# Kernel tuning notes

Hardware: AMD Instinct MI355X
Metric: run time of the kernel (lower is better)

The kernel has to match this reference:

```python
import jax, jax.numpy as jnp
import numpy as np

HIDDEN = 10

def setup_inputs() -> dict:
    key = jax.random.key(0)
    ks = jax.random.split(key, 12)
    B, T = 4096, 2048
    s_in = 1.0 / np.sqrt(HIDDEN)  # PyTorch RNN/Linear default init scale
    inp = {
        "x": jax.random.normal(ks[0], (B, T, 1), dtype=jnp.float32),
        "hidden_state": jax.random.normal(ks[1], (2, B, HIDDEN), dtype=jnp.float32),
        # layer 0 (input_size=1)
        "W_ih0": jax.random.uniform(ks[2], (HIDDEN, 1), jnp.float32, -s_in, s_in),
        "W_hh0": jax.random.uniform(ks[3], (HIDDEN, HIDDEN), jnp.float32, -s_in, s_in),
        "b_ih0": jax.random.uniform(ks[4], (HIDDEN,), jnp.float32, -s_in, s_in),
        "b_hh0": jax.random.uniform(ks[5], (HIDDEN,), jnp.float32, -s_in, s_in),
        # layer 1 (input_size=HIDDEN)
        "W_ih1": jax.random.uniform(ks[6], (HIDDEN, HIDDEN), jnp.float32, -s_in, s_in),
        "W_hh1": jax.random.uniform(ks[7], (HIDDEN, HIDDEN), jnp.float32, -s_in, s_in),
        "b_ih1": jax.random.uniform(ks[8], (HIDDEN,), jnp.float32, -s_in, s_in),
        "b_hh1": jax.random.uniform(ks[9], (HIDDEN,), jnp.float32, -s_in, s_in),
        # output Linear(10, 1)
        "W_out": jax.random.uniform(ks[10], (1, HIDDEN), jnp.float32, -s_in, s_in),
        "b_out": jax.random.uniform(ks[11], (1,), jnp.float32, -s_in, s_in),
    }
    return inp


def reference(x, hidden_state, W_ih0, W_hh0, b_ih0, b_hh0,
              W_ih1, W_hh1, b_ih1, b_hh1, W_out, b_out):
    # x: [B, T, 1]; hidden_state: [2, B, H]
    h0_init, h1_init = hidden_state[0], hidden_state[1]  # [B, H] each
    xs = jnp.swapaxes(x, 0, 1)  # [T, B, 1] for scan over time

    def step(carry, xt):
        h0, h1 = carry
        h0n = jnp.tanh(xt @ W_ih0.T + b_ih0 + h0 @ W_hh0.T + b_hh0)
        h1n = jnp.tanh(h0n @ W_ih1.T + b_ih1 + h1 @ W_hh1.T + b_hh1)
        return (h0n, h1n), h1n

    (h0_f, h1_f), ys = jax.lax.scan(step, (h0_init, h1_init), xs)  # ys: [T, B, H]
    rnn_output = jnp.swapaxes(ys, 0, 1)  # [B, T, H]
    outs = rnn_output @ W_out.T + b_out  # [B, T, 1] (fused per-timestep Linear)
    hidden_out = jnp.stack([h0_f, h1_f], axis=0)  # [2, B, H]
    return outs, hidden_out
```

## Files before the change

kernel.cpp:

```cpp
#include <hip/hip_runtime.h>

#define HID 10
#define TT  2048
#define BB  4096

typedef float f2 __attribute__((ext_vector_type(2)));

static __device__ __forceinline__ f2 pkmul(f2 a, f2 b) {
    f2 d; asm("v_pk_mul_f32 %0, %1, %2" : "=v"(d) : "v"(a), "v"(b)); return d;
}
static __device__ __forceinline__ f2 pkfma(f2 a, f2 b, f2 c) {
    f2 d; asm("v_pk_fma_f32 %0, %1, %2, %3" : "=v"(d) : "v"(a), "v"(b), "v"(c)); return d;
}

__device__ __forceinline__ float fast_tanh(float x) {
    float e = exp2f(x * 2.885390081777926814f);
    float r = __builtin_amdgcn_rcpf(e + 1.0f);
    return fmaf(-2.0f, r, 1.0f);
}

__global__ void __launch_bounds__(128) rnn_kernel(
    const float* __restrict__ x,    const float* __restrict__ hs,
    const float* __restrict__ Wih0, const float* __restrict__ Whh0,
    const float* __restrict__ bih0, const float* __restrict__ bhh0,
    const float* __restrict__ Wih1, const float* __restrict__ Whh1,
    const float* __restrict__ bih1, const float* __restrict__ bhh1,
    const float* __restrict__ Wout, const float* __restrict__ boutp,
    float* __restrict__ out)
{
    const int tid   = threadIdx.x;
    const bool isA  = tid < 64;
    const int lane  = tid & 15;
    const int grp   = (tid >> 4) & 3;
    const int row   = blockIdx.x * 4 + grp;
    const bool act  = (lane < HID);
    const bool olane = (lane == HID);

    __shared__ float lds[4 * 144];
    float* ring = &lds[grp * 144];
    float* h1b  = &lds[grp * 144 + 128];

    const float* xrow = x   + (size_t)row * TT;
    float*       orow = out + (size_t)row * TT;

    f2 whh0p[5]; float wih0i = 0.f, b0c = 0.f;
    f2 H0[5];
    float4 xq = make_float4(0.f, 0.f, 0.f, 0.f);
    float h0own = 0.f;
    f2 wih1p[5], whh1p[5]; float b1c = 0.f;
    f2 H1[5];
    float h1own = 0.f;
    float P1 = 0.f, P2 = 0.f, P3 = 0.f;

    if (isA) {
        #pragma unroll
        for (int j = 0; j < 5; ++j)
            whh0p[j] = act ? f2{Whh0[lane*HID + 2*j], Whh0[lane*HID + 2*j+1]}
                           : f2{0.f, 0.f};
        wih0i = act ? Wih0[lane] : 0.f;
        b0c   = act ? (bih0[lane] + bhh0[lane]) : 0.f;
        #pragma unroll
        for (int j = 0; j < 5; ++j)
            H0[j] = f2{hs[row*HID + 2*j], hs[row*HID + 2*j+1]};
        xq = *(const float4*)(xrow);
    } else {
        #pragma unroll
        for (int j = 0; j < 5; ++j) {
            wih1p[j] = act ? f2{Wih1[lane*HID + 2*j], Wih1[lane*HID + 2*j+1]}
                           : f2{0.f, 0.f};
            whh1p[j] = act ? f2{Whh1[lane*HID + 2*j], Whh1[lane*HID + 2*j+1]}
                     : (olane ? f2{Wout[2*j], Wout[2*j+1]} : f2{0.f, 0.f});
        }
        b1c = act ? (bih1[lane] + bhh1[lane]) : (olane ? boutp[0] : 0.f);
        #pragma unroll
        for (int j = 0; j < 5; ++j)
            H1[j] = f2{hs[BB*HID + row*HID + 2*j], hs[BB*HID + row*HID + 2*j+1]};
    }

    for (int m = 0; m <= TT / 4; ++m) {
        if (isA) {
            if (m < TT / 4) {
                const int mn = (m + 1 < TT / 4) ? m + 1 : m;
                const float4 xn = *(const float4*)(xrow + 4 * mn);
                const float xs[4] = {xq.x, xq.y, xq.z, xq.w};
                #pragma unroll
                for (int k = 0; k < 4; ++k) {
                    const int i = 4 * m + k;
                    f2 acc = pkmul(whh0p[0], H0[0]);
                    acc = pkfma(whh0p[1], H0[1], acc);
                    acc = pkfma(whh0p[2], H0[2], acc);
                    acc = pkfma(whh0p[3], H0[3], acc);
                    acc = pkfma(whh0p[4], H0[4], acc);
                    const float a0 = fmaf(xs[k], wih0i, b0c);
                    h0own = fast_tanh((a0 + acc.x) + acc.y);
                    ring[(i & 7) * 16 + lane] = h0own;
                    __builtin_amdgcn_wave_barrier();
                    const float* rb = &ring[(i & 7) * 16];
                    const float4 r0 = *(const float4*)(rb);
                    const float4 r1 = *(const float4*)(rb + 4);
                    const f2     r2 = *(const f2*)(rb + 8);
                    H0[0] = f2{r0.x, r0.y}; H0[1] = f2{r0.z, r0.w};
                    H0[2] = f2{r1.x, r1.y}; H0[3] = f2{r1.z, r1.w};
                    H0[4] = r2;
                }
                xq = xn;
            }
        } else {
            if (m > 0) {
                const int tb = 4 * (m - 1);
                f2 hb[4][5];
                #pragma unroll
                for (int k = 0; k < 4; ++k) {
                    const float* rb = &ring[((tb + k) & 7) * 16];
                    const float4 r0 = *(const float4*)(rb);
                    const float4 r1 = *(const float4*)(rb + 4);
                    const f2     r2 = *(const f2*)(rb + 8);
                    hb[k][0] = f2{r0.x, r0.y}; hb[k][1] = f2{r0.z, r0.w};
                    hb[k][2] = f2{r1.x, r1.y}; hb[k][3] = f2{r1.z, r1.w};
                    hb[k][4] = r2;
                }
                float c0 = 0.f, c1 = 0.f, c2 = 0.f, c3 = 0.f;
                #pragma unroll
                for (int k = 0; k < 4; ++k) {
                    f2 bcc = pkmul(wih1p[0], hb[k][0]);
                    bcc = pkfma(wih1p[1], hb[k][1], bcc);
                    bcc = pkfma(wih1p[2], hb[k][2], bcc);
                    bcc = pkfma(wih1p[3], hb[k][3], bcc);
                    bcc = pkfma(wih1p[4], hb[k][4], bcc);
                    bcc = pkfma(whh1p[0], H1[0], bcc);
                    bcc = pkfma(whh1p[1], H1[1], bcc);
                    bcc = pkfma(whh1p[2], H1[2], bcc);
                    bcc = pkfma(whh1p[3], H1[3], bcc);
                    bcc = pkfma(whh1p[4], H1[4], bcc);
                    const float s1 = (b1c + bcc.x) + bcc.y;
                    if      (k == 0) c0 = s1;
                    else if (k == 1) c1 = s1;
                    else if (k == 2) c2 = s1;
                    else             c3 = s1;
                    h1own = fast_tanh(s1);
                    h1b[lane] = h1own;
                    __builtin_amdgcn_wave_barrier();
                    const float4 q0 = *(const float4*)(h1b);
                    const float4 q1 = *(const float4*)(h1b + 4);
                    const f2     q2 = *(const f2*)(h1b + 8);
                    H1[0] = f2{q0.x, q0.y}; H1[1] = f2{q0.z, q0.w};
                    H1[2] = f2{q1.x, q1.y}; H1[3] = f2{q1.z, q1.w};
                    H1[4] = q2;
                }
                if (olane && m >= 2)
                    *(float4*)(orow + tb - 4) = make_float4(P1, P2, P3, c0);
                P1 = c1; P2 = c2; P3 = c3;
            }
        }
        __syncthreads();
    }

    if (!isA) {
        f2 cc = pkmul(whh1p[0], H1[0]);
        cc = pkfma(whh1p[1], H1[1], cc);
        cc = pkfma(whh1p[2], H1[2], cc);
        cc = pkfma(whh1p[3], H1[3], cc);
        cc = pkfma(whh1p[4], H1[4], cc);
        const float ofin = (b1c + cc.x) + cc.y;
        if (olane)
            *(float4*)(orow + TT - 4) = make_float4(P1, P2, P3, ofin);
    }

    if (isA) {
        if (act) out[(size_t)BB*TT + (size_t)row*HID + lane] = h0own;
    } else {
        if (act) out[(size_t)BB*TT + (size_t)BB*HID + (size_t)row*HID + lane] = h1own;
    }
}

extern "C" void kernel_launch(void* const* d_in, const int* in_sizes, int n_in,
                              void* d_out, int out_size, void* d_ws, size_t ws_size,
                              hipStream_t stream) {
    const float* x    = (const float*)d_in[0];
    const float* hs   = (const float*)d_in[1];
    const float* Wih0 = (const float*)d_in[2];
    const float* Whh0 = (const float*)d_in[3];
    const float* bih0 = (const float*)d_in[4];
    const float* bhh0 = (const float*)d_in[5];
    const float* Wih1 = (const float*)d_in[6];
    const float* Whh1 = (const float*)d_in[7];
    const float* bih1 = (const float*)d_in[8];
    const float* bhh1 = (const float*)d_in[9];
    const float* Wout = (const float*)d_in[10];
    const float* bout = (const float*)d_in[11];
    float* out = (float*)d_out;

    dim3 grid(BB / 4), block(128);
    hipLaunchKernelGGL(rnn_kernel, grid, block, 0, stream,
        x, hs, Wih0, Whh0, bih0, bhh0, Wih1, Whh1, bih1, bhh1, Wout, bout, out);
}
```

Baseline: 298.1 us.

## Interleave two independent batch rows per thread group to hide recurrence latency

Each 16-lane group now advances two batch rows instead of one, interleaving their serial recurrence steps so that the dependency chains (packed FMAs, tanh, LDS exchange) of one row can overlap with the other's. The grid is halved and the LDS ring buffers are doubled to match. This is meant to raise instruction-level parallelism in a latency-bound sequential loop, at the cost of more registers per thread and half as many blocks in flight.

```diff
diff --git a/kernel.cpp b/kernel.cpp
--- a/kernel.cpp
+++ b/kernel.cpp
@@ -32,25 +32,28 @@
     const bool isA  = tid < 64;
     const int lane  = tid & 15;
     const int grp   = (tid >> 4) & 3;
-    const int row   = blockIdx.x * 4 + grp;
+    const int row0  = blockIdx.x * 8 + grp;
+    const int row1  = row0 + 4;
     const bool act  = (lane < HID);
     const bool olane = (lane == HID);
 
-    __shared__ float lds[4 * 144];
-    float* ring = &lds[grp * 144];
-    float* h1b  = &lds[grp * 144 + 128];
-
-    const float* xrow = x   + (size_t)row * TT;
-    float*       orow = out + (size_t)row * TT;
-
-    f2 whh0p[5]; float wih0i = 0.f, b0c = 0.f;
-    f2 H0[5];
-    float4 xq = make_float4(0.f, 0.f, 0.f, 0.f);
-    float h0own = 0.f;
-    f2 wih1p[5], whh1p[5]; float b1c = 0.f;
-    f2 H1[5];
-    float h1own = 0.f;
-    float P1 = 0.f, P2 = 0.f, P3 = 0.f;
+    __shared__ float lds[8 * 144];
+    float* ring0 = &lds[grp * 144];
+    float* ring1 = &lds[(grp + 4) * 144];
+    float* h1b0  = ring0 + 128;
+    float* h1b1  = ring1 + 128;
+
+    const float* x0 = x + (size_t)row0 * TT;
+    const float* x1 = x + (size_t)row1 * TT;
+    float*       o0 = out + (size_t)row0 * TT;
+    float*       o1 = out + (size_t)row1 * TT;
+
+    f2 whh0p[5]; float wih0i = 0.f, bc = 0.f;
+    f2 wih1p[5], whh1p[5];
+    f2 H_0[5], H_1[5];
+    float4 xq0 = make_float4(0,0,0,0), xq1 = make_float4(0,0,0,0);
+    float own0 = 0.f, own1 = 0.f;
+    float P10=0.f,P20=0.f,P30=0.f, P11=0.f,P21=0.f,P31=0.f;
 
     if (isA) {
         #pragma unroll
@@ -58,11 +61,14 @@
             whh0p[j] = act ? f2{Whh0[lane*HID + 2*j], Whh0[lane*HID + 2*j+1]}
                            : f2{0.f, 0.f};
         wih0i = act ? Wih0[lane] : 0.f;
-        b0c   = act ? (bih0[lane] + bhh0[lane]) : 0.f;
-        #pragma unroll
-        for (int j = 0; j < 5; ++j)
-            H0[j] = f2{hs[row*HID + 2*j], hs[row*HID + 2*j+1]};
-        xq = *(const float4*)(xrow);
+        bc    = act ? (bih0[lane] + bhh0[lane]) : 0.f;
+        #pragma unroll
+        for (int j = 0; j < 5; ++j) {
+            H_0[j] = f2{hs[row0*HID + 2*j], hs[row0*HID + 2*j+1]};
+            H_1[j] = f2{hs[row1*HID + 2*j], hs[row1*HID + 2*j+1]};
+        }
+        xq0 = *(const float4*)(x0);
+        xq1 = *(const float4*)(x1);
     } else {
         #pragma unroll
         for (int j = 0; j < 5; ++j) {
@@ -71,106 +77,139 @@
             whh1p[j] = act ? f2{Whh1[lane*HID + 2*j], Whh1[lane*HID + 2*j+1]}
                      : (olane ? f2{Wout[2*j], Wout[2*j+1]} : f2{0.f, 0.f});
         }
-        b1c = act ? (bih1[lane] + bhh1[lane]) : (olane ? boutp[0] : 0.f);
-        #pragma unroll
-        for (int j = 0; j < 5; ++j)
-            H1[j] = f2{hs[BB*HID + row*HID + 2*j], hs[BB*HID + row*HID + 2*j+1]};
-    }
-
-    for (int m = 0; m <= TT / 4; ++m) {
+        bc = act ? (bih1[lane] + bhh1[lane]) : (olane ? boutp[0] : 0.f);
+        #pragma unroll
+        for (int j = 0; j < 5; ++j) {
+            H_0[j] = f2{hs[BB*HID + row0*HID + 2*j], hs[BB*HID + row0*HID + 2*j+1]};
+            H_1[j] = f2{hs[BB*HID + row1*HID + 2*j], hs[BB*HID + row1*HID + 2*j+1]};
+        }
+    }
+
+#define ASTEP(HV, RING, XV, OWN) do {                                    \
+    f2 acc = pkmul(whh0p[0], HV[0]);                                     \
+    acc = pkfma(whh0p[1], HV[1], acc);                                   \
+    acc = pkfma(whh0p[2], HV[2], acc);                                   \
+    acc = pkfma(whh0p[3], HV[3], acc);                                   \
+    acc = pkfma(whh0p[4], HV[4], acc);                                   \
+    const float a0 = fmaf((XV), wih0i, bc);                              \
+    OWN = fast_tanh((a0 + acc.x) + acc.y);                               \
+    (RING)[slot + lane] = OWN;                                           \
+    __builtin_amdgcn_wave_barrier();                                     \
+    const float* _rb = (RING) + slot;                                    \
+    const float4 _r0 = *(const float4*)(_rb);                            \
+    const float4 _r1 = *(const float4*)(_rb + 4);                        \
+    const f2     _r2 = *(const f2*)(_rb + 8);                            \
+    HV[0] = f2{_r0.x, _r0.y}; HV[1] = f2{_r0.z, _r0.w};                  \
+    HV[2] = f2{_r1.x, _r1.y}; HV[3] = f2{_r1.z, _r1.w};                  \
+    HV[4] = _r2;                                                         \
+} while (0)
+
+#define BSTEP(HV, H1B, U0, U1, U2, OWN, SDST) do {                       \
+    f2 qc = pkmul(whh1p[0], HV[0]);                                      \
+    qc = pkfma(whh1p[1], HV[1], qc);                                     \
+    qc = pkfma(whh1p[2], HV[2], qc);                                     \
+    qc = pkfma(whh1p[3], HV[3], qc);                                     \
+    qc = pkfma(whh1p[4], HV[4], qc);                                     \
+    f2 pc = pkmul(wih1p[0], f2{U0.x, U0.y});                             \
+    pc = pkfma(wih1p[1], f2{U0.z, U0.w}, pc);                            \
+    pc = pkfma(wih1p[2], f2{U1.x, U1.y}, pc);                            \
+    pc = pkfma(wih1p[3], f2{U1.z, U1.w}, pc);                            \
+    pc = pkfma(wih1p[4], U2, pc);                                        \
+    const float _s1 = ((bc + qc.x) + qc.y) + (pc.x + pc.y);              \
+    SDST = _s1;                                    \
+    OWN = fast_tanh(_s1);                                                \
+    (H1B)[lane] = OWN;                                                   \
+    __builtin_amdgcn_wave_barrier();                                     \
+    const float4 _q0 = *(const float4*)(H1B);                            \
+    const float4 _q1 = *(const float4*)((H1B) + 4);                      \
+    const f2     _q2 = *(const f2*)((H1B) + 8);                          \
+    HV[0] = f2{_q0.x, _q0.y}; HV[1] = f2{_q0.z, _q0.w};                  \
+    HV[2] = f2{_q1.x, _q1.y}; HV[3] = f2{_q1.z, _q1.w};                  \
+    HV[4] = _q2;                                                         \
+} while (0)
+
+    const int M = TT / 4;
+    for (int m = 0; m <= M; ++m) {
         if (isA) {
-            if (m < TT / 4) {
-                const int mn = (m + 1 < TT / 4) ? m + 1 : m;
-                const float4 xn = *(const float4*)(xrow + 4 * mn);
-                const float xs[4] = {xq.x, xq.y, xq.z, xq.w};
+            if (m < M) {
+                const int mn = (m + 1 < M) ? m + 1 : M - 1;
+                const float4 xn0 = *(const float4*)(x0 + 4 * mn);
+                const float4 xn1 = *(const float4*)(x1 + 4 * mn);
+                const float xs0[4] = {xq0.x, xq0.y, xq0.z, xq0.w};
+                const float xs1[4] = {xq1.x, xq1.y, xq1.z, xq1.w};
                 #pragma unroll
                 for (int k = 0; k < 4; ++k) {
-                    const int i = 4 * m + k;
-                    f2 acc = pkmul(whh0p[0], H0[0]);
-                    acc = pkfma(whh0p[1], H0[1], acc);
-                    acc = pkfma(whh0p[2], H0[2], acc);
-                    acc = pkfma(whh0p[3], H0[3], acc);
-                    acc = pkfma(whh0p[4], H0[4], acc);
-                    const float a0 = fmaf(xs[k], wih0i, b0c);
-                    h0own = fast_tanh((a0 + acc.x) + acc.y);
-                    ring[(i & 7) * 16 + lane] = h0own;
-                    __builtin_amdgcn_wave_barrier();
-                    const float* rb = &ring[(i & 7) * 16];
-                    const float4 r0 = *(const float4*)(rb);
-                    const float4 r1 = *(const float4*)(rb + 4);
-                    const f2     r2 = *(const f2*)(rb + 8);
-                    H0[0] = f2{r0.x, r0.y}; H0[1] = f2{r0.z, r0.w};
-                    H0[2] = f2{r1.x, r1.y}; H0[3] = f2{r1.z, r1.w};
-                    H0[4] = r2;
+                    const int slot = ((4 * m + k) & 7) * 16;
+                    ASTEP(H_0, ring0, xs0[k], own0);
+                    ASTEP(H_1, ring1, xs1[k], own1);
                 }
-                xq = xn;
+                xq0 = xn0; xq1 = xn1;
             }
         } else {
             if (m > 0) {
                 const int tb = 4 * (m - 1);
-                f2 hb[4][5];
+                float c00=0.f,c10=0.f,c20=0.f,c30=0.f;
+                float c01=0.f,c11=0.f,c21=0.f,c31=0.f;
                 #pragma unroll
                 for (int k = 0; k < 4; ++k) {
-                    const float* rb = &ring[((tb + k) & 7) * 16];
-                    const float4 r0 = *(const float4*)(rb);
-                    const float4 r1 = *(const float4*)(rb + 4);
-                    const f2     r2 = *(const f2*)(rb + 8);
-                    hb[k][0] = f2{r0.x, r0.y}; hb[k][1] = f2{r0.z, r0.w};
-                    hb[k][2] = f2{r1.x, r1.y}; hb[k][3] = f2{r1.z, r1.w};
-                    hb[k][4] = r2;
+                    const int slot = ((tb + k) & 7) * 16;
+                    const float* rb0 = ring0 + slot;
+                    const float* rb1 = ring1 + slot;
+                    const float4 u0 = *(const float4*)(rb0);
+                    const float4 u1 = *(const float4*)(rb0 + 4);
+                    const f2     u2 = *(const f2*)(rb0 + 8);
+                    const float4 v0 = *(const float4*)(rb1);
+                    const float4 v1 = *(const float4*)(rb1 + 4);
+                    const f2     v2 = *(const f2*)(rb1 + 8);
+                    float s0d, s1d;
+                    BSTEP(H_0, h1b0, u0, u1, u2, own0, s0d);
+                    BSTEP(H_1, h1b1, v0, v1, v2, own1, s1d);
+                    if      (k == 0) { c00 = s0d; c01 = s1d; }
+                    else if (k == 1) { c10 = s0d; c11 = s1d; }
+                    else if (k == 2) { c20 = s0d; c21 = s1d; }
+                    else             { c30 = s0d; c31 = s1d; }
                 }
-                float c0 = 0.f, c1 = 0.f, c2 = 0.f, c3 = 0.f;
-                #pragma unroll
-                for (int k = 0; k < 4; ++k) {
-                    f2 bcc = pkmul(wih1p[0], hb[k][0]);
-                    bcc = pkfma(wih1p[1], hb[k][1], bcc);
-                    bcc = pkfma(wih1p[2], hb[k][2], bcc);
-                    bcc = pkfma(wih1p[3], hb[k][3], bcc);
-                    bcc = pkfma(wih1p[4], hb[k][4], bcc);
-                    bcc = pkfma(whh1p[0], H1[0], bcc);
-                    bcc = pkfma(whh1p[1], H1[1], bcc);
-                    bcc = pkfma(whh1p[2], H1[2], bcc);
-                    bcc = pkfma(whh1p[3], H1[3], bcc);
-                    bcc = pkfma(whh1p[4], H1[4], bcc);
-                    const float s1 = (b1c + bcc.x) + bcc.y;
-                    if      (k == 0) c0 = s1;
-                    else if (k == 1) c1 = s1;
-                    else if (k == 2) c2 = s1;
-                    else             c3 = s1;
-                    h1own = fast_tanh(s1);
-                    h1b[lane] = h1own;
-                    __builtin_amdgcn_wave_barrier();
-                    const float4 q0 = *(const float4*)(h1b);
-                    const float4 q1 = *(const float4*)(h1b + 4);
-                    const f2     q2 = *(const f2*)(h1b + 8);
-                    H1[0] = f2{q0.x, q0.y}; H1[1] = f2{q0.z, q0.w};
-                    H1[2] = f2{q1.x, q1.y}; H1[3] = f2{q1.z, q1.w};
-                    H1[4] = q2;
+                if (olane && m >= 2) {
+                    *(float4*)(o0 + tb - 4) = make_float4(P10, P20, P30, c00);
+                    *(float4*)(o1 + tb - 4) = make_float4(P11, P21, P31, c01);
                 }
-                if (olane && m >= 2)
-                    *(float4*)(orow + tb - 4) = make_float4(P1, P2, P3, c0);
-                P1 = c1; P2 = c2; P3 = c3;
+                P10 = c10; P20 = c20; P30 = c30;
+                P11 = c11; P21 = c21; P31 = c31;
             }
         }
         __syncthreads();
     }
 
     if (!isA) {
-        f2 cc = pkmul(whh1p[0], H1[0]);
-        cc = pkfma(whh1p[1], H1[1], cc);
-        cc = pkfma(whh1p[2], H1[2], cc);
-        cc = pkfma(whh1p[3], H1[3], cc);
-        cc = pkfma(whh1p[4], H1[4], cc);
-        const float ofin = (b1c + cc.x) + cc.y;
-        if (olane)
-            *(float4*)(orow + TT - 4) = make_float4(P1, P2, P3, ofin);
+        f2 e0 = pkmul(whh1p[0], H_0[0]);
+        e0 = pkfma(whh1p[1], H_0[1], e0);
+        e0 = pkfma(whh1p[2], H_0[2], e0);
+        e0 = pkfma(whh1p[3], H_0[3], e0);
+        e0 = pkfma(whh1p[4], H_0[4], e0);
+        f2 e1 = pkmul(whh1p[0], H_1[0]);
+        e1 = pkfma(whh1p[1], H_1[1], e1);
+        e1 = pkfma(whh1p[2], H_1[2], e1);
+        e1 = pkfma(whh1p[3], H_1[3], e1);
+        e1 = pkfma(whh1p[4], H_1[4], e1);
+        if (olane) {
+            *(float4*)(o0 + TT - 4) = make_float4(P10, P20, P30, (bc + e0.x) + e0.y);
+            *(float4*)(o1 + TT - 4) = make_float4(P11, P21, P31, (bc + e1.x) + e1.y);
+        }
     }
 
     if (isA) {
-        if (act) out[(size_t)BB*TT + (size_t)row*HID + lane] = h0own;
+        if (act) {
+            out[(size_t)BB*TT + (size_t)row0*HID + lane] = own0;
+            out[(size_t)BB*TT + (size_t)row1*HID + lane] = own1;
+        }
     } else {
-        if (act) out[(size_t)BB*TT + (size_t)BB*HID + (size_t)row*HID + lane] = h1own;
-    }
+        if (act) {
+            out[(size_t)BB*TT + (size_t)BB*HID + (size_t)row0*HID + lane] = own0;
+            out[(size_t)BB*TT + (size_t)BB*HID + (size_t)row1*HID + lane] = own1;
+        }
+    }
+#undef ASTEP
+#undef BSTEP
 }
 
 extern "C" void kernel_launch(void* const* d_in, const int* in_sizes, int n_in,
@@ -190,7 +229,7 @@
     const float* bout = (const float*)d_in[11];
     float* out = (float*)d_out;
 
-    dim3 grid(BB / 4), block(128);
+    dim3 grid(BB / 8), block(128);
     hipLaunchKernelGGL(rnn_kernel, grid, block, 0, stream,
         x, hs, Wih0, Whh0, bih0, bhh0, Wih1, Whh1, bih1, bhh1, Wout, bout, out);
 }
```

Measured after the change: 487.9 us. 63.7% more time.

## Split layer-1 into input-projection and recurrent waves for a three-stage pipeline

Applied to the files above, without the earlier changes.

Adds a third wavefront per block. The new wave computes the non-recurrent W_ih1·h0 projection plus bias for each timestep and passes it through an LDS ring to the recurrent wave. The recurrent layer-1 wave then runs only the 5-step W_hh1·h1 chain per timestep, which balances it with the layer-0 wave and shortens the critical dependency chain. The costs are two extra pipeline iterations of block-wide barriers, more LDS, and 192-thread blocks that change occupancy.

```diff
diff --git a/kernel.cpp b/kernel.cpp
--- a/kernel.cpp
+++ b/kernel.cpp
@@ -19,7 +19,7 @@
     return fmaf(-2.0f, r, 1.0f);
 }
 
-__global__ void __launch_bounds__(128) rnn_kernel(
+__global__ void __launch_bounds__(192) rnn_kernel(
     const float* __restrict__ x,    const float* __restrict__ hs,
     const float* __restrict__ Wih0, const float* __restrict__ Whh0,
     const float* __restrict__ bih0, const float* __restrict__ bhh0,
@@ -29,73 +29,76 @@
     float* __restrict__ out)
 {
     const int tid   = threadIdx.x;
-    const bool isA  = tid < 64;
+    const int role  = tid >> 6;
     const int lane  = tid & 15;
     const int grp   = (tid >> 4) & 3;
     const int row   = blockIdx.x * 4 + grp;
     const bool act  = (lane < HID);
     const bool olane = (lane == HID);
 
-    __shared__ float lds[4 * 144];
-    float* ring = &lds[grp * 144];
-    float* h1b  = &lds[grp * 144 + 128];
+    __shared__ float lds[4 * 272];
+    float* h0r = &lds[grp * 272];
+    float* ur  = h0r + 128;
+    float* h1b = h0r + 256;
 
     const float* xrow = x   + (size_t)row * TT;
     float*       orow = out + (size_t)row * TT;
 
-    f2 whh0p[5]; float wih0i = 0.f, b0c = 0.f;
-    f2 H0[5];
-    float4 xq = make_float4(0.f, 0.f, 0.f, 0.f);
-    float h0own = 0.f;
-    f2 wih1p[5], whh1p[5]; float b1c = 0.f;
-    f2 H1[5];
-    float h1own = 0.f;
+    f2 w0p[5]; float wih0i = 0.f, b0c = 0.f; f2 H0[5];
+    float4 xq = make_float4(0,0,0,0);
+    f2 w1p[5]; float ub = 0.f;
+    f2 w2p[5]; f2 H1[5]; float bo = 0.f;
     float P1 = 0.f, P2 = 0.f, P3 = 0.f;
-
-    if (isA) {
-        #pragma unroll
-        for (int j = 0; j < 5; ++j)
-            whh0p[j] = act ? f2{Whh0[lane*HID + 2*j], Whh0[lane*HID + 2*j+1]}
-                           : f2{0.f, 0.f};
+    float h0own = 0.f, h1own = 0.f;
+
+    if (role == 0) {
+        #pragma unroll
+        for (int j = 0; j < 5; ++j)
+            w0p[j] = act ? f2{Whh0[lane*HID + 2*j], Whh0[lane*HID + 2*j+1]}
+                         : f2{0.f, 0.f};
         wih0i = act ? Wih0[lane] : 0.f;
         b0c   = act ? (bih0[lane] + bhh0[lane]) : 0.f;
         #pragma unroll
         for (int j = 0; j < 5; ++j)
             H0[j] = f2{hs[row*HID + 2*j], hs[row*HID + 2*j+1]};
         xq = *(const float4*)(xrow);
+    } else if (role == 1) {
+        #pragma unroll
+        for (int j = 0; j < 5; ++j)
+            w1p[j] = act ? f2{Wih1[lane*HID + 2*j], Wih1[lane*HID + 2*j+1]}
+                         : f2{0.f, 0.f};
+        ub = act ? (bih1[lane] + bhh1[lane]) : (olane ? boutp[0] : 0.f);
     } else {
         #pragma unroll
-        for (int j = 0; j < 5; ++j) {
-            wih1p[j] = act ? f2{Wih1[lane*HID + 2*j], Wih1[lane*HID + 2*j+1]}
-                           : f2{0.f, 0.f};
-            whh1p[j] = act ? f2{Whh1[lane*HID + 2*j], Whh1[lane*HID + 2*j+1]}
-                     : (olane ? f2{Wout[2*j], Wout[2*j+1]} : f2{0.f, 0.f});
-        }
-        b1c = act ? (bih1[lane] + bhh1[lane]) : (olane ? boutp[0] : 0.f);
+        for (int j = 0; j < 5; ++j)
+            w2p[j] = act ? f2{Whh1[lane*HID + 2*j], Whh1[lane*HID + 2*j+1]}
+                   : (olane ? f2{Wout[2*j], Wout[2*j+1]} : f2{0.f, 0.f});
         #pragma unroll
         for (int j = 0; j < 5; ++j)
             H1[j] = f2{hs[BB*HID + row*HID + 2*j], hs[BB*HID + row*HID + 2*j+1]};
+        bo = boutp[0];
     }
 
-    for (int m = 0; m <= TT / 4; ++m) {
-        if (isA) {
-            if (m < TT / 4) {
-                const int mn = (m + 1 < TT / 4) ? m + 1 : m;
+    const int M = TT / 4;
+    for (int m = 0; m <= M + 1; ++m) {
+        if (role == 0) {
+            if (m < M) {
+                const int mn = (m + 1 < M) ? m + 1 : M - 1;
                 const float4 xn = *(const float4*)(xrow + 4 * mn);
                 const float xs[4] = {xq.x, xq.y, xq.z, xq.w};
                 #pragma unroll
                 for (int k = 0; k < 4; ++k) {
-                    const int i = 4 * m + k;
-                    f2 acc = pkmul(whh0p[0], H0[0]);
-                    acc = pkfma(whh0p[1], H0[1], acc);
-                    acc = pkfma(whh0p[2], H0[2], acc);
-                    acc = pkfma(whh0p[3], H0[3], acc);
-                    acc = pkfma(whh0p[4], H0[4], acc);
+                    const int slot = ((4 * m + k) & 7) * 16;
+                    f2 acc = pkmul(w0p[0], H0[0]);
+                    acc = pkfma(w0p[1], H0[1], acc);
+                    acc = pkfma(w0p[2], H0[2], acc);
+                    acc = pkfma(w0p[3], H0[3], acc);
+                    acc = pkfma(w0p[4], H0[4], acc);
                     const float a0 = fmaf(xs[k], wih0i, b0c);
                     h0own = fast_tanh((a0 + acc.x) + acc.y);
-                    ring[(i & 7) * 16 + lane] = h0own;
+                    h0r[slot + lane] = h0own;
                     __builtin_amdgcn_wave_barrier();
-                    const float* rb = &ring[(i & 7) * 16];
+                    const float* rb = h0r + slot;
                     const float4 r0 = *(const float4*)(rb);
                     const float4 r1 = *(const float4*)(rb + 4);
                     const f2     r2 = *(const f2*)(rb + 8);
@@ -105,34 +108,43 @@
                 }
                 xq = xn;
             }
+        } else if (role == 1) {
+            if (m >= 1 && m <= M) {
+                const int tb = 4 * (m - 1);
+                float4 a[4], b[4]; f2 c[4];
+                #pragma unroll
+                for (int k = 0; k < 4; ++k) {
+                    const float* rb = h0r + ((tb + k) & 7) * 16;
+                    a[k] = *(const float4*)(rb);
+                    b[k] = *(const float4*)(rb + 4);
+                    c[k] = *(const f2*)(rb + 8);
+                }
+                #pragma unroll
+                for (int k = 0; k < 4; ++k) {
+                    f2 pc = pkmul(w1p[0], f2{a[k].x, a[k].y});
+                    pc = pkfma(w1p[1], f2{a[k].z, a[k].w}, pc);
+                    pc = pkfma(w1p[2], f2{b[k].x, b[k].y}, pc);
+                    pc = pkfma(w1p[3], f2{b[k].z, b[k].w}, pc);
+                    pc = pkfma(w1p[4], c[k], pc);
+                    ur[((tb + k) & 7) * 16 + lane] = (ub + pc.x) + pc.y;
+                }
+            }
         } else {
-            if (m > 0) {
-                const int tb = 4 * (m - 1);
-                f2 hb[4][5];
-                #pragma unroll
-                for (int k = 0; k < 4; ++k) {
-                    const float* rb = &ring[((tb + k) & 7) * 16];
-                    const float4 r0 = *(const float4*)(rb);
-                    const float4 r1 = *(const float4*)(rb + 4);
-                    const f2     r2 = *(const f2*)(rb + 8);
-                    hb[k][0] = f2{r0.x, r0.y}; hb[k][1] = f2{r0.z, r0.w};
-                    hb[k][2] = f2{r1.x, r1.y}; hb[k][3] = f2{r1.z, r1.w};
-                    hb[k][4] = r2;
-                }
+            if (m >= 2 && m <= M + 1) {
+                const int tb = 4 * (m - 2);
+                float uo[4];
+                #pragma unroll
+                for (int k = 0; k < 4; ++k)
+                    uo[k] = ur[((tb + k) & 7) * 16 + lane];
                 float c0 = 0.f, c1 = 0.f, c2 = 0.f, c3 = 0.f;
                 #pragma unroll
                 for (int k = 0; k < 4; ++k) {
-                    f2 bcc = pkmul(wih1p[0], hb[k][0]);
-                    bcc = pkfma(wih1p[1], hb[k][1], bcc);
-                    bcc = pkfma(wih1p[2], hb[k][2], bcc);
-                    bcc = pkfma(wih1p[3], hb[k][3], bcc);
-                    bcc = pkfma(wih1p[4], hb[k][4], bcc);
-                    bcc = pkfma(whh1p[0], H1[0], bcc);
-                    bcc = pkfma(whh1p[1], H1[1], bcc);
-                    bcc = pkfma(whh1p[2], H1[2], bcc);
-                    bcc = pkfma(whh1p[3], H1[3], bcc);
-                    bcc = pkfma(whh1p[4], H1[4], bcc);
-                    const float s1 = (b1c + bcc.x) + bcc.y;
+                    f2 qc = pkmul(w2p[0], H1[0]);
+                    qc = pkfma(w2p[1], H1[1], qc);
+                    qc = pkfma(w2p[2], H1[2], qc);
+                    qc = pkfma(w2p[3], H1[3], qc);
+                    qc = pkfma(w2p[4], H1[4], qc);
+                    const float s1 = (uo[k] + qc.x) + qc.y;
                     if      (k == 0) c0 = s1;
                     else if (k == 1) c1 = s1;
                     else if (k == 2) c2 = s1;
@@ -147,7 +159,7 @@
                     H1[2] = f2{q1.x, q1.y}; H1[3] = f2{q1.z, q1.w};
                     H1[4] = q2;
                 }
-                if (olane && m >= 2)
+                if (olane && m >= 3)
                     *(float4*)(orow + tb - 4) = make_float4(P1, P2, P3, c0);
                 P1 = c1; P2 = c2; P3 = c3;
             }
@@ -155,22 +167,19 @@
         __syncthreads();
     }
 
-    if (!isA) {
-        f2 cc = pkmul(whh1p[0], H1[0]);
-        cc = pkfma(whh1p[1], H1[1], cc);
-        cc = pkfma(whh1p[2], H1[2], cc);
-        cc = pkfma(whh1p[3], H1[3], cc);
-        cc = pkfma(whh1p[4], H1[4], cc);
-        const float ofin = (b1c + cc.x) + cc.y;
+    if (role == 2) {
+        f2 e = pkmul(w2p[0], H1[0]);
+        e = pkfma(w2p[1], H1[1], e);
+        e = pkfma(w2p[2], H1[2], e);
+        e = pkfma(w2p[3], H1[3], e);
+        e = pkfma(w2p[4], H1[4], e);
         if (olane)
-            *(float4*)(orow + TT - 4) = make_float4(P1, P2, P3, ofin);
+            *(float4*)(orow + TT - 4) = make_float4(P1, P2, P3, (bo + e.x) + e.y);
+        if (act)
+            out[(size_t)BB*TT + (size_t)BB*HID + (size_t)row*HID + lane] = h1own;
     }
-
-    if (isA) {
-        if (act) out[(size_t)BB*TT + (size_t)row*HID + lane] = h0own;
-    } else {
-        if (act) out[(size_t)BB*TT + (size_t)BB*HID + (size_t)row*HID + lane] = h1own;
-    }
+    if (role == 0 && act)
+        out[(size_t)BB*TT + (size_t)row*HID + lane] = h0own;
 }
 
 extern "C" void kernel_launch(void* const* d_in, const int* in_sizes, int n_in,
@@ -190,7 +199,7 @@
     const float* bout = (const float*)d_in[11];
     float* out = (float*)d_out;
 
-    dim3 grid(BB / 4), block(128);
+    dim3 grid(BB / 4), block(192);
     hipLaunchKernelGGL(rnn_kernel, grid, block, 0, stream,
         x, hs, Wih0, Whh0, bih0, bhh0, Wih1, Whh1, bih1, bhh1, Wout, bout, out);
 }
```

Result: no change. 294.0 us (-1.4%).
